# Kernel optimization log

Measured on AMD Instinct MI355X. Metric: run time of the kernel, lower is better.

## Reference

```python
import jax, jax.numpy as jnp
import numpy as np

D_MODEL = 512
N_HEADS = 8
MAX_DEPTH = 4
D_FF = 4 * D_MODEL
B, L = 4, 2048


def setup_inputs() -> dict:
    key = jax.random.key(0)
    ks = jax.random.split(key, 16)
    s = 0.02
    inp = {
        "x": jax.random.normal(ks[0], (B, L, D_MODEL), dtype=jnp.float32),
        # attention pre-norm
        "ln1_g": jnp.ones((D_MODEL,), jnp.float32),
        "ln1_b": jnp.zeros((D_MODEL,), jnp.float32),
        # MultiheadAttention in_proj (3D, D) and out_proj (D, D), torch (out, in) layout
        "Wqkv": jax.random.normal(ks[1], (3 * D_MODEL, D_MODEL), jnp.float32) * s,
        "bqkv": jnp.zeros((3 * D_MODEL,), jnp.float32),
        "Wo": jax.random.normal(ks[2], (D_MODEL, D_MODEL), jnp.float32) * s,
        "bo": jnp.zeros((D_MODEL,), jnp.float32),
        # FFN pre-norm + MLP
        "ln2_g": jnp.ones((D_MODEL,), jnp.float32),
        "ln2_b": jnp.zeros((D_MODEL,), jnp.float32),
        "W1": jax.random.normal(ks[3], (D_FF, D_MODEL), jnp.float32) * s,
        "b1": jnp.zeros((D_FF,), jnp.float32),
        "W2": jax.random.normal(ks[4], (D_MODEL, D_FF), jnp.float32) * s,
        "b2": jnp.zeros((D_MODEL,), jnp.float32),
        # token-choice depth router: LayerNorm + Linear(D,D) + GELU + Linear(D,max_depth)
        "rn_g": jnp.ones((D_MODEL,), jnp.float32),
        "rn_b": jnp.zeros((D_MODEL,), jnp.float32),
        "Rw1": jax.random.normal(ks[5], (D_MODEL, D_MODEL), jnp.float32) * s,
        "Rb1": jnp.zeros((D_MODEL,), jnp.float32),
        "Rw2": jax.random.normal(ks[6], (MAX_DEPTH, D_MODEL), jnp.float32) * s,
        "Rb2": jnp.zeros((MAX_DEPTH,), jnp.float32),
    }
    return inp


def _layernorm(x, g, b, eps=1e-5):
    mu = jnp.mean(x, axis=-1, keepdims=True)
    var = jnp.var(x, axis=-1, keepdims=True)
    return (x - mu) * jax.lax.rsqrt(var + eps) * g + b


def _block(x, ln1_g, ln1_b, Wqkv, bqkv, Wo, bo, ln2_g, ln2_b, W1, b1, W2, b2):
    Bb, Ll, D = x.shape
    H = N_HEADS
    dh = D // H
    # pre-norm self-attention
    h = _layernorm(x, ln1_g, ln1_b)
    qkv = h @ Wqkv.T + bqkv                      # (B, L, 3D)
    q, k, v = jnp.split(qkv, 3, axis=-1)
    q = q.reshape(Bb, Ll, H, dh)
    k = k.reshape(Bb, Ll, H, dh)
    v = v.reshape(Bb, Ll, H, dh)
    scores = jnp.einsum("blhd,bmhd->bhlm", q, k) / jnp.sqrt(jnp.float32(dh))
    attn = jax.nn.softmax(scores, axis=-1)
    o = jnp.einsum("bhlm,bmhd->blhd", attn, v).reshape(Bb, Ll, D)
    x = x + (o @ Wo.T + bo)
    # pre-norm FFN (exact-erf GELU, matching torch nn.GELU default)
    h2 = _layernorm(x, ln2_g, ln2_b)
    f = jax.nn.gelu(h2 @ W1.T + b1, approximate=False) @ W2.T + b2
    return x + f


def reference(x, ln1_g, ln1_b, Wqkv, bqkv, Wo, bo, ln2_g, ln2_b, W1, b1, W2, b2,
              rn_g, rn_b, Rw1, Rb1, Rw2, Rb2):
    # --- token-choice depth router (eval mode: argmax) ---
    rh = _layernorm(x, rn_g, rn_b)
    rh = jax.nn.gelu(rh @ Rw1.T + Rb1, approximate=False)
    router_logits = rh @ Rw2.T + Rb2             # (B, L, MAX_DEPTH)
    depths = jnp.argmax(router_logits, axis=-1) + 1  # (B, L) in [1, MAX_DEPTH]
    # --- dense recursion with torch.where-style selection ---
    cur = x
    for level in range(1, MAX_DEPTH + 1):
        upd = _block(cur, ln1_g, ln1_b, Wqkv, bqkv, Wo, bo,
                     ln2_g, ln2_b, W1, b1, W2, b2)
        keep = (depths >= level)[..., None]      # (B, L, 1)
        cur = jnp.where(keep, upd, cur)
    return cur, depths, router_logits
```

## Files before the change

kernel.cpp:

```cpp
#include <hip/hip_runtime.h>

typedef unsigned short u16;
typedef __attribute__((ext_vector_type(8))) short short8;
typedef __attribute__((ext_vector_type(4))) short s16x4;
typedef __attribute__((ext_vector_type(4))) float floatx4;
typedef __attribute__((ext_vector_type(4))) unsigned short u16x4;

#define NTOK 8192
#define DMODEL 512
#define DFF 2048
#define LSEQ 2048

__device__ __forceinline__ u16 f2bf(float f) {
    union { float f; unsigned u; } x; x.f = f;
    unsigned r = (x.u + 0x7fffu + ((x.u >> 16) & 1u)) >> 16;
    return (u16)r;
}

__device__ __forceinline__ float geluf(float x) {
    return 0.5f * x * (1.0f + erff(x * 0.70710678118654752f));
}

__device__ __forceinline__ void gload_lds16(const void* g, void* l) {
    __builtin_amdgcn_global_load_lds(
        (const __attribute__((address_space(1))) void*)g,
        (__attribute__((address_space(3))) void*)l,
        16, 0, 0);
}

__device__ __forceinline__ s16x4 pack_p(float p0, float p1, float p2, float p3) {
    union { float f; unsigned u; } a{p0}, b{p1}, c{p2}, d{p3};
    union { unsigned u[2]; s16x4 s; } r;
    r.u[0] = (a.u >> 16) | (b.u & 0xffff0000u);
    r.u[1] = (c.u >> 16) | (d.u & 0xffff0000u);
    return r.s;
}

__global__ __launch_bounds__(256) void cvt_w(const float* __restrict__ wq,
                                             const float* __restrict__ wo,
                                             const float* __restrict__ w1,
                                             const float* __restrict__ w2,
                                             u16* __restrict__ out) {
    int i = blockIdx.x * 256 + threadIdx.x;
    float v;
    if (i < 786432)       v = wq[i];
    else if (i < 1048576) v = wo[i - 786432];
    else if (i < 2097152) v = w1[i - 1048576];
    else                  v = w2[i - 2097152];
    out[i] = f2bf(v);
}

__global__ __launch_bounds__(256) void copy_f32(const float* __restrict__ a,
                                                float* __restrict__ b) {
    size_t i = ((size_t)blockIdx.x * 256 + threadIdx.x) * 4;
    *(floatx4*)&b[i] = *(const floatx4*)&a[i];
}

template<bool OUTF32>
__global__ __launch_bounds__(256)
void ln_k(const float* __restrict__ x, const float* __restrict__ g,
          const float* __restrict__ bb, void* __restrict__ outp) {
    const int row = blockIdx.x * 4 + (threadIdx.x >> 6);
    const int lane = threadIdx.x & 63;
    const float* xr = x + (size_t)row * DMODEL;
    const int c0 = lane * 4, c1 = c0 + 256;
    floatx4 a = *(const floatx4*)&xr[c0];
    floatx4 b = *(const floatx4*)&xr[c1];
    float s = 0.f, sq = 0.f;
#pragma unroll
    for (int e = 0; e < 4; ++e) { s += a[e]; sq += a[e] * a[e]; }
#pragma unroll
    for (int e = 0; e < 4; ++e) { s += b[e]; sq += b[e] * b[e]; }
#pragma unroll
    for (int m = 32; m >= 1; m >>= 1) {
        s += __shfl_xor(s, m);
        sq += __shfl_xor(sq, m);
    }
    const float mean = s * (1.f / 512.f);
    const float rstd = rsqrtf(sq * (1.f / 512.f) - mean * mean + 1e-5f);
    floatx4 g0 = *(const floatx4*)&g[c0];
    floatx4 g1 = *(const floatx4*)&g[c1];
    floatx4 b0 = *(const floatx4*)&bb[c0];
    floatx4 b1 = *(const floatx4*)&bb[c1];
    floatx4 y0, y1;
#pragma unroll
    for (int e = 0; e < 4; ++e) {
        y0[e] = (a[e] - mean) * rstd * g0[e] + b0[e];
        y1[e] = (b[e] - mean) * rstd * g1[e] + b1[e];
    }
    if (OUTF32) {
        float* o = (float*)outp + (size_t)row * DMODEL;
        *(floatx4*)&o[c0] = y0;
        *(floatx4*)&o[c1] = y1;
    } else {
        u16* o = (u16*)outp + (size_t)row * DMODEL;
        u16x4 p0, p1;
#pragma unroll
        for (int e = 0; e < 4; ++e) { p0[e] = f2bf(y0[e]); p1[e] = f2bf(y1[e]); }
        *(u16x4*)&o[c0] = p0;
        *(u16x4*)&o[c1] = p1;
    }
}

template<int EPI, int BN>
__global__ __launch_bounds__(256, 2)
void gemm_bt(const u16* __restrict__ A, const u16* __restrict__ Bw,
             const float* __restrict__ bias,
             u16* __restrict__ Cb, float* __restrict__ Cf,
             const float* __restrict__ res, const float* __restrict__ depth,
             float aux, int N, int K) {
    constexpr int NJ = BN / 32;
    __shared__ __align__(16) u16 As[128 * 32];
    __shared__ __align__(16) u16 Bs[BN * 32];
    const int tid = threadIdx.x;
    const int lane = tid & 63;
    const int w = tid >> 6;
    const int wm = (w >> 1) * 64;
    const int wn = (w & 1) * (BN / 2);
    const int mBase = blockIdx.x * 128;
    const int nBase = blockIdx.y * BN;
    const int q4 = lane >> 4, rl = lane & 15;

    floatx4 acc[4][NJ];
#pragma unroll
    for (int i = 0; i < 4; ++i)
#pragma unroll
        for (int j = 0; j < NJ; ++j) acc[i][j] = (floatx4){0.f, 0.f, 0.f, 0.f};

    const int i0 = tid, i1 = tid + 256;
    const int ar0 = i0 >> 2, ac0 = ((i0 & 3) ^ ((i0 >> 3) & 3)) * 8;
    const int ar1 = i1 >> 2, ac1 = ((i1 & 3) ^ ((i1 >> 3) & 3)) * 8;
    const u16* pA0 = A + (size_t)(mBase + ar0) * K + ac0;
    const u16* pA1 = A + (size_t)(mBase + ar1) * K + ac1;
    const u16* pB0 = Bw + (size_t)(nBase + ar0) * K + ac0;
    const u16* pB1 = (BN == 128) ? Bw + (size_t)(nBase + ar1) * K + ac1 : pB0;
    u16* lA0 = &As[i0 * 8];
    u16* lA1 = &As[i1 * 8];
    u16* lB0 = &Bs[i0 * 8];
    u16* lB1 = (BN == 128) ? &Bs[i1 * 8] : lB0;

    for (int k0 = 0; k0 < K; k0 += 32) {
        gload_lds16(pA0, lA0);
        gload_lds16(pA1, lA1);
        gload_lds16(pB0, lB0);
        if (BN == 128) gload_lds16(pB1, lB1);
        pA0 += 32; pA1 += 32; pB0 += 32;
        if (BN == 128) pB1 += 32;
        __syncthreads();
        short8 af[4], bf[NJ];
#pragma unroll
        for (int t = 0; t < 4; ++t) {
            const int r = wm + t * 16 + rl;
            af[t] = *(const short8*)&As[r * 32 + (q4 ^ ((r >> 1) & 3)) * 8];
        }
#pragma unroll
        for (int t = 0; t < NJ; ++t) {
            const int r = wn + t * 16 + rl;
            bf[t] = *(const short8*)&Bs[r * 32 + (q4 ^ ((r >> 1) & 3)) * 8];
        }
#pragma unroll
        for (int ti = 0; ti < 4; ++ti)
#pragma unroll
            for (int tj = 0; tj < NJ; ++tj)
                acc[ti][tj] = __builtin_amdgcn_mfma_f32_16x16x32_bf16(
                    af[ti], bf[tj], acc[ti][tj], 0, 0, 0);
        __syncthreads();
    }

#pragma unroll
    for (int ti = 0; ti < 4; ++ti) {
        const int r0 = mBase + wm + ti * 16 + q4 * 4;
#pragma unroll
        for (int tj = 0; tj < NJ; ++tj) {
            const int c = nBase + wn + tj * 16 + rl;
            const float bv = bias[c];
#pragma unroll
            for (int rr = 0; rr < 4; ++rr) {
                const int r = r0 + rr;
                float v = acc[ti][tj][rr] + bv;
                if (EPI == 0) {
                    if (c < 512) v *= aux;
                    Cb[(size_t)r * N + c] = f2bf(v);
                } else if (EPI == 1) {
                    Cb[(size_t)r * N + c] = f2bf(geluf(v));
                } else if (EPI == 2) {
                    Cf[(size_t)r * N + c] = res[(size_t)r * N + c] + v;
                } else {
                    if (depth[r] >= aux)
                        Cf[(size_t)r * N + c] = res[(size_t)r * N + c] + v;
                }
            }
        }
    }
}

__global__ __launch_bounds__(256, 2)
void attn_k(const u16* __restrict__ qkv, u16* __restrict__ o) {
    const int qt = blockIdx.x;
    const int bh = blockIdx.y;
    const int b = bh >> 3, h = bh & 7;
    const int tid = threadIdx.x, lane = tid & 63, w = tid >> 6;
    const int tok0 = b * LSEQ;
    const int qrow0 = qt * 128 + w * 32;
    const int q4 = lane >> 4, rl = lane & 15;

    __shared__ __align__(16) u16 Kt[128 * 64];
    __shared__ __align__(16) u16 Vt[64 * 132];

    short8 qf[2][2];
#pragma unroll
    for (int nt = 0; nt < 2; ++nt)
#pragma unroll
        for (int ks = 0; ks < 2; ++ks)
            qf[nt][ks] = *(const short8*)&qkv[(size_t)(tok0 + qrow0 + nt * 16 + rl) * 1536
                                              + h * 64 + ks * 32 + q4 * 8];

    floatx4 oacc[4][2];
#pragma unroll
    for (int dt = 0; dt < 4; ++dt)
#pragma unroll
        for (int nt = 0; nt < 2; ++nt) oacc[dt][nt] = (floatx4){0.f, 0.f, 0.f, 0.f};
    float lsum[2] = {0.f, 0.f};

    for (int kt = 0; kt < 16; ++kt) {
        const int kv0 = kt * 128;
        __syncthreads();
#pragma unroll
        for (int it = 0; it < 4; ++it) {
            const int i = it * 256 + tid;
            const int r = i >> 3;
            const int c = ((i & 7) ^ (r & 7)) * 8;
            gload_lds16(&qkv[(size_t)(tok0 + kv0 + r) * 1536 + 512 + h * 64 + c],
                        &Kt[i * 8]);
        }
        {
            const int c = tid & 63;
            const int r0 = (tid >> 6) * 4;
#pragma unroll
            for (int it = 0; it < 8; ++it) {
                const int r = r0 + it * 16;
                const u16* vp = &qkv[(size_t)(tok0 + kv0 + r) * 1536 + 1024 + h * 64 + c];
                u16x4 pk;
                pk[0] = vp[0]; pk[1] = vp[1536]; pk[2] = vp[3072]; pk[3] = vp[4608];
                *(u16x4*)&Vt[c * 132 + r] = pk;
            }
        }
        __syncthreads();

#pragma unroll
        for (int mt = 0; mt < 8; ++mt) {
            const int r = mt * 16 + rl;
            short8 kf0 = *(const short8*)&Kt[r * 64 + ((q4) ^ (r & 7)) * 8];
            short8 kf1 = *(const short8*)&Kt[r * 64 + ((4 + q4) ^ (r & 7)) * 8];
            floatx4 s[2];
#pragma unroll
            for (int nt = 0; nt < 2; ++nt) {
                s[nt] = __builtin_amdgcn_mfma_f32_16x16x32_bf16(kf0, qf[nt][0],
                        (floatx4){0.f, 0.f, 0.f, 0.f}, 0, 0, 0);
                s[nt] = __builtin_amdgcn_mfma_f32_16x16x32_bf16(kf1, qf[nt][1],
                        s[nt], 0, 0, 0);
            }
            s16x4 pb[2];
#pragma unroll
            for (int nt = 0; nt < 2; ++nt) {
                const float p0 = exp2f(s[nt][0]);
                const float p1 = exp2f(s[nt][1]);
                const float p2 = exp2f(s[nt][2]);
                const float p3 = exp2f(s[nt][3]);
                lsum[nt] += (p0 + p1) + (p2 + p3);
                pb[nt] = pack_p(p0, p1, p2, p3);
            }
#pragma unroll
            for (int dt = 0; dt < 4; ++dt) {
                s16x4 vf = *(const s16x4*)&Vt[(dt * 16 + rl) * 132 + mt * 16 + q4 * 4];
#pragma unroll
                for (int nt = 0; nt < 2; ++nt)
                    oacc[dt][nt] = __builtin_amdgcn_mfma_f32_16x16x16bf16_1k(
                        vf, pb[nt], oacc[dt][nt], 0, 0, 0);
            }
        }
    }

#pragma unroll
    for (int nt = 0; nt < 2; ++nt) {
        float l = lsum[nt];
        l += __shfl_xor(l, 16);
        l += __shfl_xor(l, 32);
        const float inv = 1.0f / l;
        const size_t row = tok0 + qrow0 + nt * 16 + rl;
#pragma unroll
        for (int dt = 0; dt < 4; ++dt) {
            u16x4 pk;
#pragma unroll
            for (int rr = 0; rr < 4; ++rr) pk[rr] = f2bf(oacc[dt][nt][rr] * inv);
            *(u16x4*)&o[row * DMODEL + h * 64 + dt * 16 + q4 * 4] = pk;
        }
    }
}

__global__ __launch_bounds__(256)
void router_gemm1(const float* __restrict__ A, const float* __restrict__ W,
                  const float* __restrict__ bias, float* __restrict__ out) {
    __shared__ double At[32][67];
    __shared__ double Bt[32][67];
    const int tid = threadIdx.x;
    const int tx = tid & 15, ty = tid >> 4;
    const int mb = blockIdx.x * 64, nb = blockIdx.y * 64;
    double acc[4][4] = {};
    for (int k0 = 0; k0 < 512; k0 += 32) {
#pragma unroll
        for (int i = 0; i < 8; ++i) {
            const int e = tid + i * 256;
            const int r = e >> 5, c = e & 31;
            At[c][r] = (double)A[(size_t)(mb + r) * 512 + k0 + c];
            Bt[c][r] = (double)W[(size_t)(nb + r) * 512 + k0 + c];
        }
        __syncthreads();
#pragma unroll 4
        for (int kk = 0; kk < 32; ++kk) {
            double av[4], bv[4];
#pragma unroll
            for (int i = 0; i < 4; ++i) av[i] = At[kk][ty * 4 + i];
#pragma unroll
            for (int j = 0; j < 4; ++j) bv[j] = Bt[kk][tx * 4 + j];
#pragma unroll
            for (int i = 0; i < 4; ++i)
#pragma unroll
                for (int j = 0; j < 4; ++j)
                    acc[i][j] = fma(av[i], bv[j], acc[i][j]);
        }
        __syncthreads();
    }
#pragma unroll
    for (int i = 0; i < 4; ++i) {
        const int r = mb + ty * 4 + i;
#pragma unroll
        for (int j = 0; j < 4; ++j) {
            const int c = nb + tx * 4 + j;
            out[(size_t)r * 512 + c] = geluf((float)(acc[i][j] + (double)bias[c]));
        }
    }
}

__global__ __launch_bounds__(256)
void router_logits_k(const float* __restrict__ rr, const float* __restrict__ Rw2,
                     const float* __restrict__ Rb2, float* __restrict__ logits,
                     float* __restrict__ depthf) {
    const int t = blockIdx.x * 4 + (threadIdx.x >> 6);
    const int lane = threadIdx.x & 63;
    const float* xr = rr + (size_t)t * 512;
    const int c0 = lane * 4, c1 = c0 + 256;
    floatx4 a = *(const floatx4*)&xr[c0];
    floatx4 b = *(const floatx4*)&xr[c1];
    double s[4];
#pragma unroll
    for (int d = 0; d < 4; ++d) {
        const float* wr = Rw2 + d * 512;
        floatx4 wa = *(const floatx4*)&wr[c0];
        floatx4 wb = *(const floatx4*)&wr[c1];
        double acc = 0.0;
#pragma unroll
        for (int e = 0; e < 4; ++e) acc += (double)a[e] * (double)wa[e];
#pragma unroll
        for (int e = 0; e < 4; ++e) acc += (double)b[e] * (double)wb[e];
        s[d] = acc;
    }
#pragma unroll
    for (int m = 32; m >= 1; m >>= 1)
#pragma unroll
        for (int d = 0; d < 4; ++d) s[d] += __shfl_xor(s[d], m);
    if (lane == 0) {
        double bv = -1e300;
        int best = 0;
#pragma unroll
        for (int d = 0; d < 4; ++d) {
            const double v = s[d] + (double)Rb2[d];
            logits[(size_t)t * 4 + d] = (float)v;
            if (v > bv) { bv = v; best = d; }
        }
        depthf[t] = (float)(best + 1);
    }
}

extern "C" void kernel_launch(void* const* d_in, const int* in_sizes, int n_in,
                              void* d_out, int out_size, void* d_ws, size_t ws_size,
                              hipStream_t stream) {
    (void)in_sizes; (void)n_in; (void)out_size; (void)ws_size;
    const float* x    = (const float*)d_in[0];
    const float* ln1g = (const float*)d_in[1];
    const float* ln1b = (const float*)d_in[2];
    const float* Wqkv = (const float*)d_in[3];
    const float* bqkv = (const float*)d_in[4];
    const float* Wo   = (const float*)d_in[5];
    const float* bo   = (const float*)d_in[6];
    const float* ln2g = (const float*)d_in[7];
    const float* ln2b = (const float*)d_in[8];
    const float* W1   = (const float*)d_in[9];
    const float* b1   = (const float*)d_in[10];
    const float* W2   = (const float*)d_in[11];
    const float* b2   = (const float*)d_in[12];
    const float* rng  = (const float*)d_in[13];
    const float* rnb  = (const float*)d_in[14];
    const float* Rw1  = (const float*)d_in[15];
    const float* Rb1  = (const float*)d_in[16];
    const float* Rw2  = (const float*)d_in[17];
    const float* Rb2  = (const float*)d_in[18];

    float* cur    = (float*)d_out;
    float* depthf = cur + (size_t)NTOK * DMODEL;
    float* logits = depthf + NTOK;

    char* ws = (char*)d_ws;
    float* xmid = (float*)ws;
    u16* sbuf   = (u16*)(ws + 16777216);
    u16* qkvb   = (u16*)(ws + 25165824);
    u16* ffb    = (u16*)(ws + 50331648);
    u16* wbf    = (u16*)(ws + 83886080);
    float* rrf  = (float*)ffb;

    u16* wq = wbf;
    u16* wo = wbf + 786432;
    u16* w1 = wbf + 1048576;
    u16* w2 = wbf + 2097152;

    const float qsc = 0.125f * 1.4426950408889634f;

    cvt_w<<<12288, 256, 0, stream>>>(Wqkv, Wo, W1, W2, wbf);
    copy_f32<<<4096, 256, 0, stream>>>(x, cur);

    ln_k<true><<<2048, 256, 0, stream>>>(x, rng, rnb, xmid);
    router_gemm1<<<dim3(128, 8), 256, 0, stream>>>(xmid, Rw1, Rb1, rrf);
    router_logits_k<<<2048, 256, 0, stream>>>(rrf, Rw2, Rb2, logits, depthf);

    for (int level = 1; level <= 4; ++level) {
        ln_k<false><<<2048, 256, 0, stream>>>(cur, ln1g, ln1b, sbuf);
        gemm_bt<0, 128><<<dim3(64, 12), 256, 0, stream>>>(
            sbuf, wq, bqkv, qkvb, nullptr, nullptr, nullptr, qsc, 1536, 512);
        attn_k<<<dim3(16, 32), 256, 0, stream>>>(qkvb, sbuf);
        gemm_bt<2, 64><<<dim3(64, 8), 256, 0, stream>>>(
            sbuf, wo, bo, nullptr, xmid, cur, nullptr, 0.f, 512, 512);
        ln_k<false><<<2048, 256, 0, stream>>>(xmid, ln2g, ln2b, sbuf);
        gemm_bt<1, 128><<<dim3(64, 16), 256, 0, stream>>>(
            sbuf, w1, b1, ffb, nullptr, nullptr, nullptr, 0.f, 2048, 512);
        gemm_bt<3, 64><<<dim3(64, 8), 256, 0, stream>>>(
            ffb, w2, b2, nullptr, cur, xmid, depthf, (float)level, 512, 2048);
    }
}
```

Measured before the change: 1.133 ms.

## Widen router GEMM tile to 64x128 with float LDS and vectorized loads

Restructures the fp64 router GEMM so each block computes a 64x128 tile, giving each thread 4x8 accumulators. Shared-memory staging switches from double to float, with conversion to double at use time, and global loads become float4 vectors. The aim is more reuse per LDS load, less LDS traffic and fewer blocks for the fp64-bound router projection. The cost is higher register pressure from 32 double accumulators, and the launch bound is raised to request two blocks per CU.

```diff
diff --git a/kernel.cpp b/kernel.cpp
--- a/kernel.cpp
+++ b/kernel.cpp
@@ -298,35 +298,45 @@
     }
 }
 
-__global__ __launch_bounds__(256)
+__global__ __launch_bounds__(256, 2)
 void router_gemm1(const float* __restrict__ A, const float* __restrict__ W,
                   const float* __restrict__ bias, float* __restrict__ out) {
-    __shared__ double At[32][67];
-    __shared__ double Bt[32][67];
+    __shared__ float Af[32][68];
+    __shared__ float Bf[32][132];
     const int tid = threadIdx.x;
     const int tx = tid & 15, ty = tid >> 4;
-    const int mb = blockIdx.x * 64, nb = blockIdx.y * 64;
-    double acc[4][4] = {};
+    const int mb = blockIdx.x * 64, nb = blockIdx.y * 128;
+    double acc[4][8] = {};
     for (int k0 = 0; k0 < 512; k0 += 32) {
 #pragma unroll
-        for (int i = 0; i < 8; ++i) {
-            const int e = tid + i * 256;
-            const int r = e >> 5, c = e & 31;
-            At[c][r] = (double)A[(size_t)(mb + r) * 512 + k0 + c];
-            Bt[c][r] = (double)W[(size_t)(nb + r) * 512 + k0 + c];
+        for (int it = 0; it < 2; ++it) {
+            const int ch = tid + it * 256;
+            const int m = ch >> 3, c4 = (ch & 7) * 4;
+            const floatx4 v = *(const floatx4*)&A[(size_t)(mb + m) * 512 + k0 + c4];
+#pragma unroll
+            for (int e = 0; e < 4; ++e) Af[c4 + e][m] = v[e];
+        }
+#pragma unroll
+        for (int it = 0; it < 4; ++it) {
+            const int ch = tid + it * 256;
+            const int n = ch >> 3, c4 = (ch & 7) * 4;
+            const floatx4 v = *(const floatx4*)&W[(size_t)(nb + n) * 512 + k0 + c4];
+#pragma unroll
+            for (int e = 0; e < 4; ++e) Bf[c4 + e][n] = v[e];
         }
         __syncthreads();
 #pragma unroll 4
         for (int kk = 0; kk < 32; ++kk) {
-            double av[4], bv[4];
-#pragma unroll
-            for (int i = 0; i < 4; ++i) av[i] = At[kk][ty * 4 + i];
-#pragma unroll
-            for (int j = 0; j < 4; ++j) bv[j] = Bt[kk][tx * 4 + j];
+            const floatx4 a4 = *(const floatx4*)&Af[kk][ty * 4];
+            double av[4], bv[8];
+#pragma unroll
+            for (int i = 0; i < 4; ++i) av[i] = (double)a4[i];
+#pragma unroll
+            for (int j = 0; j < 8; ++j) bv[j] = (double)Bf[kk][tx + 16 * j];
 #pragma unroll
             for (int i = 0; i < 4; ++i)
 #pragma unroll
-                for (int j = 0; j < 4; ++j)
+                for (int j = 0; j < 8; ++j)
                     acc[i][j] = fma(av[i], bv[j], acc[i][j]);
         }
         __syncthreads();
@@ -335,8 +345,8 @@
     for (int i = 0; i < 4; ++i) {
         const int r = mb + ty * 4 + i;
 #pragma unroll
-        for (int j = 0; j < 4; ++j) {
-            const int c = nb + tx * 4 + j;
+        for (int j = 0; j < 8; ++j) {
+            const int c = nb + tx + 16 * j;
             out[(size_t)r * 512 + c] = geluf((float)(acc[i][j] + (double)bias[c]));
         }
     }
@@ -429,7 +439,7 @@
     copy_f32<<<4096, 256, 0, stream>>>(x, cur);
 
     ln_k<true><<<2048, 256, 0, stream>>>(x, rng, rnb, xmid);
-    router_gemm1<<<dim3(128, 8), 256, 0, stream>>>(xmid, Rw1, Rb1, rrf);
+    router_gemm1<<<dim3(128, 4), 256, 0, stream>>>(xmid, Rw1, Rb1, rrf);
     router_logits_k<<<2048, 256, 0, stream>>>(rrf, Rw2, Rb2, logits, depthf);
 
     for (int level = 1; level <= 4; ++level) {
```

Result: faster. 1.046 ms (-7.7%).
